# Kernel tuning notes

Hardware: AMD Instinct MI355X
Metric: run time of the kernel (lower is better)

## Reference

```python
import jax, jax.numpy as jnp
import numpy as np

NUM_EMBEDDINGS = 8192
EMBEDDING_DIM = 256
COMMITMENT_COST = 0.25


def setup_inputs() -> dict:
    key = jax.random.key(0)
    k1, k2 = jax.random.split(key)
    inputs = jax.random.normal(k1, (32, 32, 32, EMBEDDING_DIM), dtype=jnp.float32)
    # flax nn.initializers.uniform(scale=1/num_embeddings) -> U[0, scale)
    embeddings = jax.random.uniform(
        k2, (NUM_EMBEDDINGS, EMBEDDING_DIM), dtype=jnp.float32,
        minval=0.0, maxval=1.0 / NUM_EMBEDDINGS)
    return {"inputs": inputs, "embeddings": embeddings}


def reference(inputs, embeddings):
    flat_input = inputs.reshape(-1, EMBEDDING_DIM)  # [N, D]
    distances = (jnp.sum(flat_input ** 2, axis=1, keepdims=True)
                 - 2.0 * jnp.dot(flat_input, embeddings.T)
                 + jnp.sum(embeddings ** 2, axis=1)[None, :])
    encoding_indices = jnp.argmin(distances, axis=1)  # [N]
    quantized = embeddings[encoding_indices]  # [N, D]

    e_latent_loss = jnp.mean((jax.lax.stop_gradient(quantized) - flat_input) ** 2)
    q_latent_loss = jnp.mean((quantized - jax.lax.stop_gradient(flat_input)) ** 2)
    vq_loss = q_latent_loss + COMMITMENT_COST * e_latent_loss

    # straight-through estimator
    quantized_st = flat_input + jax.lax.stop_gradient(quantized - flat_input)
    quantized_st = quantized_st.reshape(inputs.shape)

    # perplexity via codebook usage histogram (avoids materializing one-hot)
    counts = jnp.zeros((NUM_EMBEDDINGS,), dtype=flat_input.dtype).at[encoding_indices].add(1.0)
    avg_probs = counts / flat_input.shape[0]
    perplexity = jnp.exp(-jnp.sum(avg_probs * jnp.log(avg_probs + 1e-10)))

    return quantized_st, vq_loss, perplexity, encoding_indices
```

## Files before the change

kernel.cpp:

```cpp
#include <hip/hip_runtime.h>
#include <math.h>

#pragma clang fp contract(off)

#define N_ROWS 32768
#define DIM    256
#define K_EMB  8192
#define BCAP   2048
#define NSUB   256

typedef float  f32x4  __attribute__((ext_vector_type(4)));
typedef short  bf16x8 __attribute__((ext_vector_type(8)));

__device__ __forceinline__ void gl_lds16(const uint4* g, uint4* l) {
  __builtin_amdgcn_global_load_lds(
      (const __attribute__((address_space(1))) unsigned int*)g,
      (__attribute__((address_space(3))) unsigned int*)l,
      16, 0, 0);
}

__device__ __forceinline__ unsigned bf_rne(float f) {
  unsigned u = __float_as_uint(f);
  return (u + 0x7fffu + ((u >> 16) & 1u)) >> 16;
}
__device__ __forceinline__ unsigned pack2(float lo, float hi) {
  return bf_rne(lo) | (bf_rne(hi) << 16);
}

__device__ __forceinline__ float np_pw128_sumsq(const float* __restrict__ a) {
  float4 v0 = *(const float4*)(a);
  float4 v1 = *(const float4*)(a + 4);
  float r0 = v0.x*v0.x, r1 = v0.y*v0.y, r2 = v0.z*v0.z, r3 = v0.w*v0.w;
  float r4 = v1.x*v1.x, r5 = v1.y*v1.y, r6 = v1.z*v1.z, r7 = v1.w*v1.w;
  for (int i = 8; i < 128; i += 8) {
    float4 w0 = *(const float4*)(a + i);
    float4 w1 = *(const float4*)(a + i + 4);
    r0 += w0.x*w0.x; r1 += w0.y*w0.y; r2 += w0.z*w0.z; r3 += w0.w*w0.w;
    r4 += w1.x*w1.x; r5 += w1.y*w1.y; r6 += w1.z*w1.z; r7 += w1.w*w1.w;
  }
  return ((r0+r1)+(r2+r3))+((r4+r5)+(r6+r7));
}

__global__ __launch_bounds__(256) void vq_sumsq(const float* __restrict__ src,
                                                float* __restrict__ dst, int nrows) {
  int gid  = blockIdx.x * 256 + threadIdx.x;
  int row  = gid >> 1, half = gid & 1;
  if (row >= nrows) return;
  float s = np_pw128_sumsq(src + (size_t)row * DIM + half * 128);
  float o = __shfl_xor(s, 1);
  if (half == 0) dst[row] = s + o;
}

__global__ __launch_bounds__(256) void vq_init(unsigned* __restrict__ hist,
                                               unsigned* __restrict__ bcnt,
                                               unsigned* __restrict__ ovf,
                                               unsigned long long* __restrict__ best) {
  int i = blockIdx.x * 256 + threadIdx.x;
  ovf[i]  = 0u;
  best[i] = ~0ull;
  if (i < K_EMB) hist[i] = 0u;
  if (i < NSUB)  bcnt[i] = 0u;
}

__global__ __launch_bounds__(256) void vq_cvt_frag(const float* __restrict__ E,
                                                   uint4* __restrict__ Eb) {
  int t = blockIdx.x * 256 + threadIdx.x;
  int tile = t >> 6, l = t & 63;
  int cfg = tile >> 3, ks = tile & 7;
  int code = cfg * 16 + (l & 15);
  int k0 = (ks * 4 + (l >> 4)) * 8;
  const float4* src = (const float4*)(E + (size_t)code * DIM + k0);
  float4 a = src[0], b = src[1];
  uint4 o;
  o.x = pack2(a.x, a.y); o.y = pack2(a.z, a.w);
  o.z = pack2(b.x, b.y); o.w = pack2(b.z, b.w);
  Eb[t] = o;
}

__global__ __launch_bounds__(256)
__attribute__((amdgpu_waves_per_eu(2, 2)))
void vq_mfma_slice(
    const float* __restrict__ X, const uint4* __restrict__ Eb,
    unsigned short* __restrict__ submax_t) {
  __shared__ __align__(16) unsigned short es[2][64 * 256];

  const int tid   = threadIdx.x;
  const int lane  = tid & 63, w = tid >> 6;
  const int lr    = lane & 15, lg = lane >> 4;
  const int wcg   = w & 1;
  const int wxg   = w >> 1;
  const int rb    = blockIdx.x >> 1;
  const int slice = blockIdx.x & 1;
  const int row0  = rb * 128;

  const uint4* ebase = Eb + (size_t)slice * 131072;

#pragma unroll
  for (int i = 0; i < 8; ++i) {
    int u = tid + i * 256;
    gl_lds16(ebase + u, ((uint4*)&es[0][0]) + u);
  }

  bf16x8 bx[4][8];
#pragma unroll
  for (int rf = 0; rf < 4; ++rf) {
    const float* xr = X + (size_t)(row0 + wxg * 64 + rf * 16 + lr) * DIM;
#pragma unroll
    for (int ks = 0; ks < 8; ++ks) {
      int k0 = (ks * 4 + lg) * 8;
      float4 a = *(const float4*)(xr + k0);
      float4 b = *(const float4*)(xr + k0 + 4);
      uint4 o;
      o.x = pack2(a.x, a.y); o.y = pack2(a.z, a.w);
      o.z = pack2(b.x, b.y); o.w = pack2(b.z, b.w);
      bx[rf][ks] = *(bf16x8*)&o;
    }
  }
  __syncthreads();

  for (int c = 0; c < 64; ++c) {
    const int cur = c & 1;
    if (c + 1 < 64) {
#pragma unroll
      for (int i = 0; i < 8; ++i) {
        int u = tid + i * 256;
        gl_lds16(ebase + (size_t)(c + 1) * 2048 + u, ((uint4*)&es[cur ^ 1][0]) + u);
      }
    }

    f32x4 acc[2][4];
#pragma unroll
    for (int ce = 0; ce < 2; ++ce)
#pragma unroll
      for (int rf = 0; rf < 4; ++rf)
        acc[ce][rf] = (f32x4){0.f, 0.f, 0.f, 0.f};

    const unsigned short* eb = &es[cur][0];
#pragma unroll
    for (int ks = 0; ks < 8; ++ks) {
      bf16x8 ev0 = *(const bf16x8*)(eb + (((wcg * 2 + 0) * 8 + ks) * 64 + lane) * 8);
      bf16x8 ev1 = *(const bf16x8*)(eb + (((wcg * 2 + 1) * 8 + ks) * 64 + lane) * 8);
#pragma unroll
      for (int rf = 0; rf < 4; ++rf) {
        acc[0][rf] = __builtin_amdgcn_mfma_f32_16x16x32_bf16(ev0, bx[rf][ks], acc[0][rf], 0, 0, 0);
        acc[1][rf] = __builtin_amdgcn_mfma_f32_16x16x32_bf16(ev1, bx[rf][ks], acc[1][rf], 0, 0, 0);
      }
    }

    const int sub = slice * 128 + c * 2 + wcg;
#pragma unroll
    for (int rf = 0; rf < 4; ++rf) {
      float m = acc[0][rf][0];
#pragma unroll
      for (int ce = 0; ce < 2; ++ce)
#pragma unroll
        for (int rg = 0; rg < 4; ++rg)
          if (ce | rg) m = fmaxf(m, acc[ce][rf][rg]);
      m = fmaxf(m, __shfl_xor(m, 16));
      m = fmaxf(m, __shfl_xor(m, 32));
      if (lg == 0) {
        int qi = (int)((m + 0.0625f) * 524288.0f);
        qi = qi < 0 ? 0 : (qi > 65535 ? 65535 : qi);
        submax_t[(size_t)sub * N_ROWS + row0 + wxg * 64 + rf * 16 + lr] =
            (unsigned short)qi;
      }
    }

    __syncthreads();
  }
}

__global__ __launch_bounds__(256) void vq_flag(
    const unsigned short* __restrict__ submax_t, const float* __restrict__ A,
    unsigned* __restrict__ bcnt, unsigned short* __restrict__ buckets,
    unsigned* __restrict__ ovf) {
  __shared__ unsigned cntA[NSUB], baseS[NSUB], cntC[NSUB];
  const int t   = threadIdx.x;
  const int row = blockIdx.x * 256 + t;
  cntA[t] = 0u; cntC[t] = 0u;
  __syncthreads();

  int mq = 0;
  for (int s = 0; s < NSUB; ++s) {
    int q = submax_t[(size_t)s * N_ROWS + row];
    mq = q > mq ? q : mq;
  }
  const int wq   = (int)((sqrtf(A[row]) * 4e-6f + 9.6e-5f) * 524288.0f) + 2;
  const int thrq = mq - wq;

  for (int s = 0; s < NSUB; ++s)
    if ((int)submax_t[(size_t)s * N_ROWS + row] >= thrq) atomicAdd(&cntA[s], 1u);
  __syncthreads();

  baseS[t] = atomicAdd(&bcnt[t], cntA[t]);
  __syncthreads();

  for (int s = 0; s < NSUB; ++s) {
    if ((int)submax_t[(size_t)s * N_ROWS + row] >= thrq) {
      unsigned p = baseS[s] + atomicAdd(&cntC[s], 1u);
      if (p < BCAP) buckets[s * BCAP + p] = (unsigned short)row;
      else          ovf[row] = 1u;
    }
  }
}

__global__ __launch_bounds__(256) void vq_exact(
    const float* __restrict__ X, const float* __restrict__ E,
    const float* __restrict__ A, const float* __restrict__ C,
    const unsigned* __restrict__ bcnt, const unsigned short* __restrict__ buckets,
    unsigned long long* __restrict__ best) {
  __shared__ float e_lds[32][260];
  __shared__ float xr[4][4][256];
  const int tid  = threadIdx.x;
  const int lane = tid & 63, w = tid >> 6;
  const int bk   = blockIdx.x >> 2, q4 = blockIdx.x & 3;

#pragma unroll
  for (int i = 0; i < 8; ++i) {
    int u = tid + i * 256;
    int code = u >> 6, koff = (u & 63) * 4;
    float4 v = *(const float4*)(E + (size_t)(bk * 32 + code) * DIM + koff);
    *(float4*)(&e_lds[code][koff]) = v;
  }
  __syncthreads();

  int n = (int)bcnt[bk]; if (n > BCAP) n = BCAP;
  const int   half = lane >> 5, c32 = lane & 31;
  const int   j  = bk * 32 + c32;
  const float cj = C[j];

  for (int p0 = q4 * 16 + w * 4; p0 < n; p0 += 64) {
    int valid[4], rows[4];
#pragma unroll
    for (int k = 0; k < 4; ++k) {
      int pk = p0 + k;
      valid[k] = (pk < n);
      rows[k]  = buckets[(size_t)bk * BCAP + (pk < n ? pk : p0)];
    }
#pragma unroll
    for (int k = 0; k < 4; ++k)
      *(float4*)(&xr[w][k][lane * 4]) =
          *(const float4*)(X + (size_t)rows[k] * DIM + lane * 4);
    asm volatile("s_waitcnt lgkmcnt(0)" ::: "memory");

    float acc0 = 0.f, acc1 = 0.f;
    const float* xa = &xr[w][half][0];
    const float* xb = &xr[w][half + 2][0];
#pragma unroll 4
    for (int kq = 0; kq < 64; ++kq) {
      float4 ev = *(const float4*)(&e_lds[c32][kq * 4]);
      float4 x0 = *(const float4*)(xa + kq * 4);
      float4 x1 = *(const float4*)(xb + kq * 4);
      acc0 = fmaf(x0.x, ev.x, acc0); acc0 = fmaf(x0.y, ev.y, acc0);
      acc0 = fmaf(x0.z, ev.z, acc0); acc0 = fmaf(x0.w, ev.w, acc0);
      acc1 = fmaf(x1.x, ev.x, acc1); acc1 = fmaf(x1.y, ev.y, acc1);
      acc1 = fmaf(x1.z, ev.z, acc1); acc1 = fmaf(x1.w, ev.w, acc1);
    }
    float d0 = (A[rows[half]]     - 2.0f * acc0) + cj;
    float d1 = (A[rows[half + 2]] - 2.0f * acc1) + cj;
    int   j0 = j, j1 = j;
#pragma unroll
    for (int mm = 1; mm < 32; mm <<= 1) {
      float od = __shfl_xor(d0, mm); int oj = __shfl_xor(j0, mm);
      if (od < d0 || (od == d0 && oj < j0)) { d0 = od; j0 = oj; }
      od = __shfl_xor(d1, mm); oj = __shfl_xor(j1, mm);
      if (od < d1 || (od == d1 && oj < j1)) { d1 = od; j1 = oj; }
    }
    if (c32 == 0) {
      if (valid[half])
        atomicMin(&best[rows[half]],
                  ((unsigned long long)__float_as_uint(d0) << 32) | (unsigned)j0);
      if (valid[half + 2])
        atomicMin(&best[rows[half + 2]],
                  ((unsigned long long)__float_as_uint(d1) << 32) | (unsigned)j1);
    }
  }
}

__global__ __launch_bounds__(256) void vq_finish(
    const float* __restrict__ X, const float* __restrict__ E,
    const float* __restrict__ A, const float* __restrict__ C,
    const unsigned* __restrict__ ovf, const unsigned long long* __restrict__ best,
    int* __restrict__ idx_out, float* __restrict__ idxf_out) {
  int row  = blockIdx.x * 4 + (threadIdx.x >> 6);
  int lane = threadIdx.x & 63;
  if (!ovf[row]) {
    if (lane == 0) {
      int j = (int)(best[row] & 0xffffffffu);
      idx_out[row]  = j;
      idxf_out[row] = (float)j;
    }
    return;
  }
  const float a_r = A[row];
  const float4* X4 = (const float4*)(X + (size_t)row * DIM);
  float bd = INFINITY; int bj = 0x7fffffff;
  for (int j = lane; j < K_EMB; j += 64) {
    const float4* E4 = (const float4*)(E + (size_t)j * DIM);
    float acc = 0.f;
    for (int kb = 0; kb < 64; ++kb) {
      float4 xv = X4[kb], ev = E4[kb];
      acc = fmaf(xv.x, ev.x, acc); acc = fmaf(xv.y, ev.y, acc);
      acc = fmaf(xv.z, ev.z, acc); acc = fmaf(xv.w, ev.w, acc);
    }
    float d = (a_r - 2.0f * acc) + C[j];
    if (d < bd || (d == bd && j < bj)) { bd = d; bj = j; }
  }
  for (int m = 1; m < 64; m <<= 1) {
    float od = __shfl_xor(bd, m);
    int   oj = __shfl_xor(bj, m);
    if (od < bd || (od == bd && oj < bj)) { bd = od; bj = oj; }
  }
  if (lane == 0) { idx_out[row] = bj; idxf_out[row] = (float)bj; }
}

__global__ __launch_bounds__(256) void vq_argmin(const float* __restrict__ X,
                                                 const float* __restrict__ E,
                                                 const float* __restrict__ A,
                                                 const float* __restrict__ C,
                                                 int* __restrict__ idx_out,
                                                 float* __restrict__ idxf_out) {
  __shared__ float4 xs4[64 * 64];
  const int tid  = threadIdx.x;
  const int rl   = tid >> 2;
  const int cg   = tid & 3;
  const int row0 = blockIdx.x * 64;

  const float4* Xg = (const float4*)(X + (size_t)row0 * DIM);
  for (int it = 0; it < 16; ++it) {
    int f4 = tid + it * 256;
    float4 v = Xg[f4];
    int r = f4 >> 6, kb = f4 & 63;
    xs4[r * 64 + (kb ^ (r & 7))] = v;
  }
  __syncthreads();

  const float a_r = A[row0 + rl];
  const int   swq = rl & 7;
  const float4* xrow = xs4 + rl * 64;

  float bd = INFINITY;
  int   bj = 0x7fffffff;

  for (int tile = 0; tile < K_EMB; tile += 16) {
    const int j0 = tile + cg * 4;
    const float4* e0 = (const float4*)(E + (size_t)(j0 + 0) * DIM);
    const float4* e1 = (const float4*)(E + (size_t)(j0 + 1) * DIM);
    const float4* e2 = (const float4*)(E + (size_t)(j0 + 2) * DIM);
    const float4* e3 = (const float4*)(E + (size_t)(j0 + 3) * DIM);
    float acc0 = 0.f, acc1 = 0.f, acc2 = 0.f, acc3 = 0.f;
#pragma unroll 4
    for (int kb = 0; kb < 64; ++kb) {
      const float4 xv = xrow[kb ^ swq];
      const float4 q0 = e0[kb], q1 = e1[kb], q2 = e2[kb], q3 = e3[kb];
      acc0 = fmaf(xv.x, q0.x, acc0); acc0 = fmaf(xv.y, q0.y, acc0);
      acc0 = fmaf(xv.z, q0.z, acc0); acc0 = fmaf(xv.w, q0.w, acc0);
      acc1 = fmaf(xv.x, q1.x, acc1); acc1 = fmaf(xv.y, q1.y, acc1);
      acc1 = fmaf(xv.z, q1.z, acc1); acc1 = fmaf(xv.w, q1.w, acc1);
      acc2 = fmaf(xv.x, q2.x, acc2); acc2 = fmaf(xv.y, q2.y, acc2);
      acc2 = fmaf(xv.z, q2.z, acc2); acc2 = fmaf(xv.w, q2.w, acc2);
      acc3 = fmaf(xv.x, q3.x, acc3); acc3 = fmaf(xv.y, q3.y, acc3);
      acc3 = fmaf(xv.z, q3.z, acc3); acc3 = fmaf(xv.w, q3.w, acc3);
    }
    const float d0 = (a_r - 2.0f * acc0) + C[j0 + 0];
    const float d1 = (a_r - 2.0f * acc1) + C[j0 + 1];
    const float d2 = (a_r - 2.0f * acc2) + C[j0 + 2];
    const float d3 = (a_r - 2.0f * acc3) + C[j0 + 3];
    if (d0 < bd) { bd = d0; bj = j0 + 0; }
    if (d1 < bd) { bd = d1; bj = j0 + 1; }
    if (d2 < bd) { bd = d2; bj = j0 + 2; }
    if (d3 < bd) { bd = d3; bj = j0 + 3; }
  }
  for (int m = 1; m < 4; m <<= 1) {
    float od = __shfl_xor(bd, m);
    int   oj = __shfl_xor(bj, m);
    if (od < bd || (od == bd && oj < bj)) { bd = od; bj = oj; }
  }
  if (cg == 0) {
    int row = row0 + rl;
    idx_out[row]  = bj;
    idxf_out[row] = (float)bj;
  }
}

__global__ __launch_bounds__(256) void vq_quant(const float* __restrict__ X,
                                                const float* __restrict__ E,
                                                const int* __restrict__ idx,
                                                float* __restrict__ out_qst,
                                                double* __restrict__ partials) {
  int gid  = blockIdx.x * 256 + threadIdx.x;
  int base = gid * 4;
  int row  = base >> 8;
  int k    = base & 255;
  int j    = idx[row];
  const float4 xv = *(const float4*)(X + (size_t)base);
  const float4 ev = *(const float4*)(E + (size_t)j * DIM + k);
  float4 o;
  float d0 = ev.x - xv.x, d1 = ev.y - xv.y, d2 = ev.z - xv.z, d3 = ev.w - xv.w;
  o.x = xv.x + d0; o.y = xv.y + d1; o.z = xv.z + d2; o.w = xv.w + d3;
  double s = (double)d0 * d0 + (double)d1 * d1 + (double)d2 * d2 + (double)d3 * d3;
  *(float4*)(out_qst + (size_t)base) = o;

  for (int m = 32; m; m >>= 1) s += __shfl_xor(s, m);
  __shared__ double wsum[4];
  int lane = threadIdx.x & 63, w = threadIdx.x >> 6;
  if (lane == 0) wsum[w] = s;
  __syncthreads();
  if (threadIdx.x == 0)
    partials[blockIdx.x] = (wsum[0] + wsum[1]) + (wsum[2] + wsum[3]);
}

__global__ void vq_zero(unsigned* counts) {
  int i = blockIdx.x * 256 + threadIdx.x;
  if (i < K_EMB) counts[i] = 0u;
}

__global__ void vq_hist(const int* __restrict__ idx, unsigned* __restrict__ counts) {
  int i = blockIdx.x * 256 + threadIdx.x;
  if (i < N_ROWS) atomicAdd(&counts[idx[i]], 1u);
}

__global__ __launch_bounds__(256) void vq_scalars(const double* __restrict__ partials,
                                                  const unsigned* __restrict__ counts,
                                                  float* __restrict__ out_loss,
                                                  float* __restrict__ out_perp) {
  __shared__ double red[256];
  int t = threadIdx.x;
  double s = 0.0;
  for (int i = t; i < 8192; i += 256) s += partials[i];
  red[t] = s;
  __syncthreads();
  for (int o = 128; o; o >>= 1) { if (t < o) red[t] += red[t + o]; __syncthreads(); }
  double mse = red[0] / (double)((size_t)N_ROWS * DIM);
  __syncthreads();

  double p = 0.0;
  for (int i = t; i < K_EMB; i += 256) {
    double pr = (double)counts[i] / (double)N_ROWS;
    p += pr * log(pr + 1e-10);
  }
  red[t] = p;
  __syncthreads();
  for (int o = 128; o; o >>= 1) { if (t < o) red[t] += red[t + o]; __syncthreads(); }
  if (t == 0) {
    float m = (float)mse;
    out_loss[0] = m + 0.25f * m;
    out_perp[0] = (float)exp(-red[0]);
  }
}

extern "C" void kernel_launch(void* const* d_in, const int* in_sizes, int n_in,
                              void* d_out, int out_size, void* d_ws, size_t ws_size,
                              hipStream_t stream) {
  const float* X = (const float*)d_in[0];
  const float* E = (const float*)d_in[1];
  float* out  = (float*)d_out;
  float* qst  = out;
  float* loss = out + 8388608;
  float* perp = out + 8388609;
  float* idxf = out + 8388610;

  float*    A        = (float*)d_ws;
  float*    C        = (float*)((char*)d_ws + 131072);
  int*      idx      = (int*)((char*)d_ws + 163840);
  unsigned* hist     = (unsigned*)((char*)d_ws + 294912);
  double*   partials = (double*)((char*)d_ws + 327680);

  vq_sumsq <<<256, 256, 0, stream>>>(X, A, N_ROWS);
  vq_sumsq <<<64,  256, 0, stream>>>(E, C, K_EMB);

  if (ws_size >= 22807552) {
    unsigned long long* best = (unsigned long long*)((char*)d_ws + 393216);
    unsigned* ovf          = (unsigned*)((char*)d_ws + 655360);
    unsigned* bcnt         = (unsigned*)((char*)d_ws + 786432);
    unsigned short* bucket = (unsigned short*)((char*)d_ws + 787456);
    uint4*    Eb           = (uint4*)((char*)d_ws + 1836032);
    unsigned short* sm     = (unsigned short*)((char*)d_ws + 6030336);

    vq_init       <<<128,  256, 0, stream>>>(hist, bcnt, ovf, best);
    vq_cvt_frag   <<<1024, 256, 0, stream>>>(E, Eb);
    vq_mfma_slice <<<512,  256, 0, stream>>>(X, Eb, sm);
    vq_flag       <<<128,  256, 0, stream>>>(sm, A, bcnt, bucket, ovf);
    vq_exact      <<<1024, 256, 0, stream>>>(X, E, A, C, bcnt, bucket, best);
    vq_finish     <<<8192, 256, 0, stream>>>(X, E, A, C, ovf, best, idx, idxf);
  } else {
    vq_zero   <<<32,  256, 0, stream>>>(hist);
    vq_argmin <<<512, 256, 0, stream>>>(X, E, A, C, idx, idxf);
  }

  vq_quant  <<<8192, 256, 0, stream>>>(X, E, idx, qst, partials);
  vq_hist   <<<128,  256, 0, stream>>>(idx, hist);
  vq_scalars<<<1,    256, 0, stream>>>(partials, hist, loss, perp);
}
```

Baseline: 358.7 us.

## Prefetch bucket rows in vq_exact, double its grid, compact vq_finish to thread-per-row

vq_exact now splits each codebook bucket across 8 blocks instead of 4 and software-prefetches the next group of bucket rows into registers while computing the current group, so global-load latency overlaps the dot-product loop. vq_finish switches from one wave per row to one thread per row, and uses a ballot to loop only over overflow rows with the full wave. This removes 8192 mostly idle block launches. It costs more registers for the prefetch buffers and an early return per wave. Overflow rows in a wave are now handled one after another.

```diff
diff --git a/kernel.cpp b/kernel.cpp
--- a/kernel.cpp
+++ b/kernel.cpp
@@ -213,7 +213,7 @@
   __shared__ float xr[4][4][256];
   const int tid  = threadIdx.x;
   const int lane = tid & 63, w = tid >> 6;
-  const int bk   = blockIdx.x >> 2, q4 = blockIdx.x & 3;
+  const int bk   = blockIdx.x >> 3, q8 = blockIdx.x & 7;
 
 #pragma unroll
   for (int i = 0; i < 8; ++i) {
@@ -229,18 +229,33 @@
   const int   j  = bk * 32 + c32;
   const float cj = C[j];
 
-  for (int p0 = q4 * 16 + w * 4; p0 < n; p0 += 64) {
-    int valid[4], rows[4];
-#pragma unroll
-    for (int k = 0; k < 4; ++k) {
-      int pk = p0 + k;
-      valid[k] = (pk < n);
-      rows[k]  = buckets[(size_t)bk * BCAP + (pk < n ? pk : p0)];
-    }
+#define LOADP(P, RW, VD, DST)                                        \
+  {                                                                  \
+    _Pragma("unroll")                                                \
+    for (int k = 0; k < 4; ++k) {                                    \
+      int pk = (P) + k;                                              \
+      VD[k] = (pk < n);                                              \
+      RW[k] = buckets[(size_t)bk * BCAP + (pk < n ? pk : (P))];      \
+      DST[k] = *(const float4*)(X + (size_t)RW[k] * DIM + lane * 4); \
+    }                                                                \
+  }
+
+  int p0 = (q8 * 4 + w) * 4;
+  if (p0 >= n) return;
+
+  int rows[4], valid[4];
+  float4 cr[4];
+  LOADP(p0, rows, valid, cr);
+
+  while (p0 < n) {
+    const int np = p0 + 128;
+    int nrows[4], nvalid[4];
+    float4 nr[4];
+    if (np < n) LOADP(np, nrows, nvalid, nr);
+
 #pragma unroll
     for (int k = 0; k < 4; ++k)
-      *(float4*)(&xr[w][k][lane * 4]) =
-          *(const float4*)(X + (size_t)rows[k] * DIM + lane * 4);
+      *(float4*)(&xr[w][k][lane * 4]) = cr[k];
     asm volatile("s_waitcnt lgkmcnt(0)" ::: "memory");
 
     float acc0 = 0.f, acc1 = 0.f;
@@ -274,7 +289,14 @@
         atomicMin(&best[rows[half + 2]],
                   ((unsigned long long)__float_as_uint(d1) << 32) | (unsigned)j1);
     }
-  }
+
+    p0 = np;
+#pragma unroll
+    for (int k = 0; k < 4; ++k) {
+      rows[k] = nrows[k]; valid[k] = nvalid[k]; cr[k] = nr[k];
+    }
+  }
+#undef LOADP
 }
 
 __global__ __launch_bounds__(256) void vq_finish(
@@ -282,36 +304,40 @@
     const float* __restrict__ A, const float* __restrict__ C,
     const unsigned* __restrict__ ovf, const unsigned long long* __restrict__ best,
     int* __restrict__ idx_out, float* __restrict__ idxf_out) {
-  int row  = blockIdx.x * 4 + (threadIdx.x >> 6);
+  int row  = blockIdx.x * 256 + threadIdx.x;
   int lane = threadIdx.x & 63;
-  if (!ovf[row]) {
-    if (lane == 0) {
-      int j = (int)(best[row] & 0xffffffffu);
-      idx_out[row]  = j;
-      idxf_out[row] = (float)j;
-    }
-    return;
-  }
-  const float a_r = A[row];
-  const float4* X4 = (const float4*)(X + (size_t)row * DIM);
-  float bd = INFINITY; int bj = 0x7fffffff;
-  for (int j = lane; j < K_EMB; j += 64) {
-    const float4* E4 = (const float4*)(E + (size_t)j * DIM);
-    float acc = 0.f;
-    for (int kb = 0; kb < 64; ++kb) {
-      float4 xv = X4[kb], ev = E4[kb];
-      acc = fmaf(xv.x, ev.x, acc); acc = fmaf(xv.y, ev.y, acc);
-      acc = fmaf(xv.z, ev.z, acc); acc = fmaf(xv.w, ev.w, acc);
-    }
-    float d = (a_r - 2.0f * acc) + C[j];
-    if (d < bd || (d == bd && j < bj)) { bd = d; bj = j; }
-  }
-  for (int m = 1; m < 64; m <<= 1) {
-    float od = __shfl_xor(bd, m);
-    int   oj = __shfl_xor(bj, m);
-    if (od < bd || (od == bd && oj < bj)) { bd = od; bj = oj; }
-  }
-  if (lane == 0) { idx_out[row] = bj; idxf_out[row] = (float)bj; }
+  unsigned o = ovf[row];
+  if (!o) {
+    int j = (int)(best[row] & 0xffffffffu);
+    idx_out[row]  = j;
+    idxf_out[row] = (float)j;
+  }
+  unsigned long long m = __ballot(o != 0u);
+  while (m) {
+    int src  = __ffsll((long long)m) - 1;
+    int orow = __shfl(row, src);
+    const float a_r = A[orow];
+    const float4* X4 = (const float4*)(X + (size_t)orow * DIM);
+    float bd = INFINITY; int bj = 0x7fffffff;
+    for (int jj = lane; jj < K_EMB; jj += 64) {
+      const float4* E4 = (const float4*)(E + (size_t)jj * DIM);
+      float acc = 0.f;
+      for (int kb = 0; kb < 64; ++kb) {
+        float4 xv = X4[kb], ev = E4[kb];
+        acc = fmaf(xv.x, ev.x, acc); acc = fmaf(xv.y, ev.y, acc);
+        acc = fmaf(xv.z, ev.z, acc); acc = fmaf(xv.w, ev.w, acc);
+      }
+      float d = (a_r - 2.0f * acc) + C[jj];
+      if (d < bd || (d == bd && jj < bj)) { bd = d; bj = jj; }
+    }
+    for (int mm = 1; mm < 64; mm <<= 1) {
+      float od = __shfl_xor(bd, mm);
+      int   oj = __shfl_xor(bj, mm);
+      if (od < bd || (od == bd && oj < bj)) { bd = od; bj = oj; }
+    }
+    if (lane == 0) { idx_out[orow] = bj; idxf_out[orow] = (float)bj; }
+    m &= m - 1;
+  }
 }
 
 __global__ __launch_bounds__(256) void vq_argmin(const float* __restrict__ X,
@@ -481,8 +507,8 @@
     vq_cvt_frag   <<<1024, 256, 0, stream>>>(E, Eb);
     vq_mfma_slice <<<512,  256, 0, stream>>>(X, Eb, sm);
     vq_flag       <<<128,  256, 0, stream>>>(sm, A, bcnt, bucket, ovf);
-    vq_exact      <<<1024, 256, 0, stream>>>(X, E, A, C, bcnt, bucket, best);
-    vq_finish     <<<8192, 256, 0, stream>>>(X, E, A, C, ovf, best, idx, idxf);
+    vq_exact      <<<2048, 256, 0, stream>>>(X, E, A, C, bcnt, bucket, best);
+    vq_finish     <<<128,  256, 0, stream>>>(X, E, A, C, ovf, best, idx, idxf);
   } else {
     vq_zero   <<<32,  256, 0, stream>>>(hist);
     vq_argmin <<<512, 256, 0, stream>>>(X, E, A, C, idx, idxf);
```

Result: slower. 380.2 us (+6.0%).
